# Optimization experiments

Hardware: AMD Instinct MI355X
Metric: run time of the kernel (lower is better)

The kernel has to match this reference:

```python
import jax, jax.numpy as jnp
import numpy as np

B, S = 4, 1024
IN_F, OUT_F = 8192, 8192
ACT_BITS = 8


def setup_inputs() -> dict:
    key = jax.random.key(0)
    k1, k2, k3, k4 = jax.random.split(key, 4)
    x = jax.random.normal(k1, (B, S, IN_F), dtype=jnp.float32)
    # each int8 byte packs two 4-bit exponent nibbles; stored as int32 values in [0, 256)
    packed_exponents = jax.random.randint(k2, (OUT_F, IN_F // 2), 0, 256, dtype=jnp.int32)
    # signs are +/-1 per weight element
    signs = jax.random.randint(k3, (OUT_F, IN_F), 0, 2, dtype=jnp.int32) * 2 - 1
    bias = jax.random.normal(k4, (OUT_F,), dtype=jnp.float32)
    activation_scale = jnp.float32(0.02)  # delta_lsb for int8 activation quant
    min_exp = -14  # python int constant (buffer min_exp in the torch module)
    return {
        "x": x,
        "packed_exponents": packed_exponents,
        "signs": signs,
        "bias": bias,
        "activation_scale": activation_scale,
        "min_exp": min_exp,
    }


def reference(x, packed_exponents, signs, bias, activation_scale, min_exp):
    q_max = 2 ** (ACT_BITS - 1) - 1   # 127
    q_min = -2 ** (ACT_BITS - 1)      # -128
    orig_shape = x.shape
    x2 = x.reshape(-1, orig_shape[-1])  # [N, IN_F]

    # int8 activation quantization (kept in float; values are exact small ints)
    a_quant = jnp.clip(jnp.round(x2 / activation_scale), q_min, q_max)

    # unpack two 4-bit exponent nibbles per byte: low nibble first, then high
    lo = packed_exponents & 0xF
    hi = (packed_exponents >> 4) & 0xF
    exps = jnp.stack([lo, hi], axis=-1).reshape(OUT_F, IN_F)  # [OUT_F, IN_F]

    # dequantized log-domain weights: sign * 2^(nibble + min_exp)
    w = signs.astype(jnp.float32) * jnp.exp2((exps + min_exp).astype(jnp.float32))

    # batched matvec (the CUDA kernel does one row of this per launch) + dequant + bias
    out = (a_quant @ w.T) * activation_scale + bias  # [N, OUT_F]
    return out.reshape(*orig_shape[:-1], OUT_F)
```

## Files before the change

### kernel.cpp

```cpp
#include <hip/hip_runtime.h>
#include <hip/hip_bf16.h>
#include <stdint.h>

#define N_TOK 4096
#define KF    8192
#define NF    8192

#define BM 256
#define BN 256
#define NT (KF / 64)
#define NKH (KF / 32)

typedef __attribute__((ext_vector_type(8))) short short8;
typedef __attribute__((ext_vector_type(4))) float f32x4;

#define GLOBAL_P(p) ((const __attribute__((address_space(1))) void*)(p))
#define LDS_P(p)    ((__attribute__((address_space(3))) void*)(p))

__global__ void quant_x(const float* __restrict__ x, const float* __restrict__ scale_p,
                        uint16_t* __restrict__ a) {
    const float s = *scale_p;
    const int n8 = N_TOK * KF / 8;
    const int stride = gridDim.x * blockDim.x;
    for (int i = blockIdx.x * blockDim.x + threadIdx.x; i < n8; i += stride) {
        const float4* xp = (const float4*)(x + (size_t)i * 8);
        float4 v0 = xp[0], v1 = xp[1];
        float q[8] = {v0.x, v0.y, v0.z, v0.w, v1.x, v1.y, v1.z, v1.w};
        union { uint16_t u16[8]; short8 v; } o;
        #pragma unroll
        for (int j = 0; j < 8; ++j) {
            float t = rintf(q[j] / s);
            t = fminf(fmaxf(t, -128.f), 127.f);
            union { float f; uint32_t u; } cv; cv.f = t;
            o.u16[j] = (uint16_t)(cv.u >> 16);
        }
        *(short8*)(a + (size_t)i * 8) = o.v;
    }
}

__global__ void dequant_w(const int* __restrict__ packed, const int* __restrict__ signs,
                          const int* __restrict__ minexp_p, uint16_t* __restrict__ w) {
    const int me = *minexp_p;
    const int ebase = (me + 127) << 7;
    const int n4 = NF * (KF / 2) / 4;
    const int stride = gridDim.x * blockDim.x;
    for (int i = blockIdx.x * blockDim.x + threadIdx.x; i < n4; i += stride) {
        int4 p  = ((const int4*)packed)[i];
        int4 s0 = ((const int4*)signs)[(size_t)i * 2];
        int4 s1 = ((const int4*)signs)[(size_t)i * 2 + 1];
        int pw[4] = {p.x, p.y, p.z, p.w};
        int sg[8] = {s0.x, s0.y, s0.z, s0.w, s1.x, s1.y, s1.z, s1.w};
        union { uint16_t u16[8]; short8 v; } o;
        #pragma unroll
        for (int j = 0; j < 4; ++j) {
            int lo = pw[j] & 0xF, hi = (pw[j] >> 4) & 0xF;
            o.u16[2 * j]     = (uint16_t)((ebase + (lo << 7)) | (sg[2 * j]     < 0 ? 0x8000 : 0));
            o.u16[2 * j + 1] = (uint16_t)((ebase + (hi << 7)) | (sg[2 * j + 1] < 0 ? 0x8000 : 0));
        }
        *(short8*)(w + (size_t)i * 8) = o.v;
    }
}

#define BARRIER()  asm volatile("s_barrier" ::: "memory")
#define WAITLGKM() asm volatile("s_waitcnt lgkmcnt(0)" ::: "memory")
#define WAITVM8()  asm volatile("s_waitcnt vmcnt(8)" ::: "memory")
#define WAITVM4()  asm volatile("s_waitcnt vmcnt(4)" ::: "memory")
#define WAITVM0()  asm volatile("s_waitcnt vmcnt(0)" ::: "memory")

__global__ __launch_bounds__(512, 2) void gemm_bt(
        const uint16_t* __restrict__ A, const uint16_t* __restrict__ W,
        const float* __restrict__ bias, const float* __restrict__ scale_p,
        float* __restrict__ out) {
    __shared__ uint16_t ldsA[4 * 256 * 32];
    __shared__ uint16_t ldsB[4 * 256 * 32];

    const int tid  = threadIdx.x;
    const int wid  = tid >> 6, lane = tid & 63;
    const int wr = wid >> 2, wc = wid & 3;
    const int rlane = lane & 15, kgrp = lane >> 4;

    const int bid = blockIdx.x;
    const int xcd = bid & 7;
    const int i_l = bid >> 3;
    const int gen = i_l >> 5;
    const int il  = i_l & 31;
    const int by  = gen * 8 + (il >> 2);
    const int bx  = xcd * 4 + (il & 3);
    const int rowA0 = by * BM;
    const int colB0 = bx * BN;

    const int o0 = tid * 16, o1 = (512 + tid) * 16;
    const int l0 = o0 ^ (((o0 >> 9) & 1) << 5);
    const int l1 = o1 ^ (((o1 >> 9) & 1) << 5);
    const char* gA0 = (const char*)A + ((size_t)(rowA0 + (l0 >> 6)) * KF) * 2 + (l0 & 63);
    const char* gA1 = (const char*)A + ((size_t)(rowA0 + (l1 >> 6)) * KF) * 2 + (l1 & 63);
    const char* gB0 = (const char*)W + ((size_t)(colB0 + (l0 >> 6)) * KF) * 2 + (l0 & 63);
    const char* gB1 = (const char*)W + ((size_t)(colB0 + (l1 >> 6)) * KF) * 2 + (l1 & 63);
    const int ldst0 = wid * 1024;
    const int ldst1 = 8192 + wid * 1024;

    int aoff[8], boff[4];
    #pragma unroll
    for (int i = 0; i < 8; ++i) {
        int row = wr * 128 + i * 16 + rlane;
        int o = row * 64 + kgrp * 16;
        aoff[i] = o ^ (((o >> 9) & 1) << 5);
    }
    #pragma unroll
    for (int n = 0; n < 4; ++n) {
        int row = wc * 64 + n * 16 + rlane;
        int o = row * 64 + kgrp * 16;
        boff[n] = o ^ (((o >> 9) & 1) << 5);
    }

#define STAGE_A(j) do { \
    char* b_ = (char*)ldsA + ((j) & 3) * 16384; \
    __builtin_amdgcn_global_load_lds(GLOBAL_P(gA0 + (size_t)(j) * 64), LDS_P(b_ + ldst0), 16, 0, 0); \
    __builtin_amdgcn_global_load_lds(GLOBAL_P(gA1 + (size_t)(j) * 64), LDS_P(b_ + ldst1), 16, 0, 0); \
} while (0)
#define STAGE_B(j) do { \
    char* b_ = (char*)ldsB + ((j) & 3) * 16384; \
    __builtin_amdgcn_global_load_lds(GLOBAL_P(gB0 + (size_t)(j) * 64), LDS_P(b_ + ldst0), 16, 0, 0); \
    __builtin_amdgcn_global_load_lds(GLOBAL_P(gB1 + (size_t)(j) * 64), LDS_P(b_ + ldst1), 16, 0, 0); \
} while (0)
#define LDA(h, slot) do { \
    const char* pa_ = (const char*)ldsA + (slot) * 16384; \
    _Pragma("unroll") for (int mm_ = 0; mm_ < 4; ++mm_) \
        afr[mm_] = *(const short8*)(pa_ + aoff[(h) * 4 + mm_]); \
} while (0)
#define LDB(slot) do { \
    const char* pb_ = (const char*)ldsB + (slot) * 16384; \
    _Pragma("unroll") for (int nn_ = 0; nn_ < 4; ++nn_) \
        bfr[nn_] = *(const short8*)(pb_ + boff[nn_]); \
} while (0)
#define MFMA_HALF(h) do { \
    __builtin_amdgcn_s_setprio(1); \
    _Pragma("unroll") for (int mm_ = 0; mm_ < 4; ++mm_) \
        _Pragma("unroll") for (int nn_ = 0; nn_ < 4; ++nn_) \
            acc[(h) * 4 + mm_][nn_] = __builtin_amdgcn_mfma_f32_16x16x32_bf16( \
                afr[mm_], bfr[nn_], acc[(h) * 4 + mm_][nn_], 0, 0, 0); \
    __builtin_amdgcn_s_setprio(0); \
} while (0)

    f32x4 acc[8][4] = {};
    short8 afr[4], bfr[4];

    STAGE_A(0); STAGE_B(0);
    STAGE_A(1); STAGE_B(1);
    STAGE_A(2); STAGE_B(2);
    WAITVM8();
    BARRIER();

    for (int t = 0; t < NT - 1; ++t) {
        const int j0 = 2 * t;
        const int s0 = j0 & 3, s1 = (j0 + 1) & 3;
        const bool g3 = (j0 + 3) < NKH;
        const bool g4 = (j0 + 4) < NKH;

        LDA(0, s0); LDB(s0);
        if (g3) STAGE_A(j0 + 3);
        BARRIER(); WAITLGKM();
        MFMA_HALF(0);
        BARRIER();
        LDA(1, s0);
        if (g3) STAGE_B(j0 + 3);
        BARRIER(); WAITLGKM();
        MFMA_HALF(1);
        WAITVM8();
        BARRIER();
        LDA(0, s1); LDB(s1);
        if (g4) STAGE_A(j0 + 4);
        BARRIER(); WAITLGKM();
        MFMA_HALF(0);
        BARRIER();
        LDA(1, s1);
        if (g4) STAGE_B(j0 + 4);
        BARRIER(); WAITLGKM();
        MFMA_HALF(1);
        if (t == NT - 2) { WAITVM4(); } else { WAITVM8(); }
        BARRIER();
    }

    {
        LDA(0, 2); LDB(2);
        BARRIER(); WAITLGKM();
        MFMA_HALF(0);
        BARRIER();
        LDA(1, 2);
        BARRIER(); WAITLGKM();
        MFMA_HALF(1);
        WAITVM0();
        BARRIER();
        LDA(0, 3); LDB(3);
        BARRIER(); WAITLGKM();
        MFMA_HALF(0);
        BARRIER();
        LDA(1, 3);
        WAITLGKM();
        MFMA_HALF(1);
    }

    const float s = *scale_p;
    const int colbase = colB0 + wc * 64 + rlane;
    const int rowbase = rowA0 + wr * 128 + kgrp * 4;
    #pragma unroll
    for (int n = 0; n < 4; ++n) {
        const float bv = bias[colbase + n * 16];
        #pragma unroll
        for (int mf = 0; mf < 8; ++mf) {
            #pragma unroll
            for (int r = 0; r < 4; ++r)
                out[(size_t)(rowbase + mf * 16 + r) * NF + colbase + n * 16] = acc[mf][n][r] * s + bv;
        }
    }
#undef STAGE_A
#undef STAGE_B
#undef LDA
#undef LDB
#undef MFMA_HALF
}

extern "C" void kernel_launch(void* const* d_in, const int* in_sizes, int n_in,
                              void* d_out, int out_size, void* d_ws, size_t ws_size,
                              hipStream_t stream) {
    const float* x      = (const float*)d_in[0];
    const int*   packed = (const int*)d_in[1];
    const int*   signs  = (const int*)d_in[2];
    const float* bias   = (const float*)d_in[3];
    const float* scale  = (const float*)d_in[4];
    const int*   minexp = (const int*)d_in[5];
    float* out = (float*)d_out;

    uint16_t* A = (uint16_t*)d_ws;
    uint16_t* W = (uint16_t*)((char*)d_ws + (size_t)N_TOK * KF * 2);

    quant_x<<<2048, 256, 0, stream>>>(x, scale, A);
    dequant_w<<<2048, 256, 0, stream>>>(packed, signs, minexp, W);
    gemm_bt<<<(N_TOK / BM) * (NF / BN), 512, 0, stream>>>(A, W, bias, scale, out);
}
```

Before: 677.8 us.

## Double-buffer LDS fragment registers to overlap LDS reads with MFMA

After: 610.4 us. 9.9% less time.

```diff
diff --git a/kernel.cpp b/kernel.cpp
--- a/kernel.cpp
+++ b/kernel.cpp
@@ -62,10 +62,11 @@
 }
 
 #define BARRIER()  asm volatile("s_barrier" ::: "memory")
-#define WAITLGKM() asm volatile("s_waitcnt lgkmcnt(0)" ::: "memory")
 #define WAITVM8()  asm volatile("s_waitcnt vmcnt(8)" ::: "memory")
 #define WAITVM4()  asm volatile("s_waitcnt vmcnt(4)" ::: "memory")
 #define WAITVM0()  asm volatile("s_waitcnt vmcnt(0)" ::: "memory")
+#define SP1 __builtin_amdgcn_s_setprio(1)
+#define SP0 __builtin_amdgcn_s_setprio(0)
 
 __global__ __launch_bounds__(512, 2) void gemm_bt(
         const uint16_t* __restrict__ A, const uint16_t* __restrict__ W,
@@ -123,82 +124,61 @@
     __builtin_amdgcn_global_load_lds(GLOBAL_P(gB0 + (size_t)(j) * 64), LDS_P(b_ + ldst0), 16, 0, 0); \
     __builtin_amdgcn_global_load_lds(GLOBAL_P(gB1 + (size_t)(j) * 64), LDS_P(b_ + ldst1), 16, 0, 0); \
 } while (0)
-#define LDA(h, slot) do { \
-    const char* pa_ = (const char*)ldsA + (slot) * 16384; \
-    _Pragma("unroll") for (int mm_ = 0; mm_ < 4; ++mm_) \
-        afr[mm_] = *(const short8*)(pa_ + aoff[(h) * 4 + mm_]); \
-} while (0)
-#define LDB(slot) do { \
-    const char* pb_ = (const char*)ldsB + (slot) * 16384; \
-    _Pragma("unroll") for (int nn_ = 0; nn_ < 4; ++nn_) \
-        bfr[nn_] = *(const short8*)(pb_ + boff[nn_]); \
-} while (0)
-#define MFMA_HALF(h) do { \
-    __builtin_amdgcn_s_setprio(1); \
+#define LDA4(DST, H, SLOT) do { \
+    const char* p_ = (const char*)ldsA + (SLOT) * 16384; \
+    _Pragma("unroll") for (int i_ = 0; i_ < 4; ++i_) \
+        DST[i_] = *(const short8*)(p_ + aoff[(H) * 4 + i_]); \
+} while (0)
+#define LDB4(DST, SLOT) do { \
+    const char* p_ = (const char*)ldsB + (SLOT) * 16384; \
+    _Pragma("unroll") for (int i_ = 0; i_ < 4; ++i_) \
+        DST[i_] = *(const short8*)(p_ + boff[i_]); \
+} while (0)
+#define MFMA16(H, AF, BF) do { \
+    SP1; \
     _Pragma("unroll") for (int mm_ = 0; mm_ < 4; ++mm_) \
         _Pragma("unroll") for (int nn_ = 0; nn_ < 4; ++nn_) \
-            acc[(h) * 4 + mm_][nn_] = __builtin_amdgcn_mfma_f32_16x16x32_bf16( \
-                afr[mm_], bfr[nn_], acc[(h) * 4 + mm_][nn_], 0, 0, 0); \
-    __builtin_amdgcn_s_setprio(0); \
+            acc[(H) * 4 + mm_][nn_] = __builtin_amdgcn_mfma_f32_16x16x32_bf16( \
+                AF[mm_], BF[nn_], acc[(H) * 4 + mm_][nn_], 0, 0, 0); \
+    SP0; \
+} while (0)
+
+#define TILE(S0, S1, S0N, ST0, ST1, ST2, ST3, VM0, VM2) do { \
+    BARRIER(); VM0; LDA4(afrY, 1, S0);                 ST0; MFMA16(0, afrX, bfrE); \
+    BARRIER();      LDA4(afrX, 0, S1); LDB4(bfrO, S1); ST1; MFMA16(1, afrY, bfrE); \
+    BARRIER(); VM2; LDA4(afrY, 1, S1);                 ST2; MFMA16(0, afrX, bfrO); \
+    BARRIER();      LDA4(afrX, 0, S0N); LDB4(bfrE, S0N); ST3; MFMA16(1, afrY, bfrO); \
 } while (0)
 
     f32x4 acc[8][4] = {};
-    short8 afr[4], bfr[4];
+    short8 afrX[4], afrY[4], bfrE[4], bfrO[4];
 
     STAGE_A(0); STAGE_B(0);
     STAGE_A(1); STAGE_B(1);
     STAGE_A(2); STAGE_B(2);
     WAITVM8();
     BARRIER();
-
-    for (int t = 0; t < NT - 1; ++t) {
-        const int j0 = 2 * t;
-        const int s0 = j0 & 3, s1 = (j0 + 1) & 3;
-        const bool g3 = (j0 + 3) < NKH;
-        const bool g4 = (j0 + 4) < NKH;
-
-        LDA(0, s0); LDB(s0);
-        if (g3) STAGE_A(j0 + 3);
-        BARRIER(); WAITLGKM();
-        MFMA_HALF(0);
-        BARRIER();
-        LDA(1, s0);
-        if (g3) STAGE_B(j0 + 3);
-        BARRIER(); WAITLGKM();
-        MFMA_HALF(1);
-        WAITVM8();
-        BARRIER();
-        LDA(0, s1); LDB(s1);
-        if (g4) STAGE_A(j0 + 4);
-        BARRIER(); WAITLGKM();
-        MFMA_HALF(0);
-        BARRIER();
-        LDA(1, s1);
-        if (g4) STAGE_B(j0 + 4);
-        BARRIER(); WAITLGKM();
-        MFMA_HALF(1);
-        if (t == NT - 2) { WAITVM4(); } else { WAITVM8(); }
-        BARRIER();
-    }
-
-    {
-        LDA(0, 2); LDB(2);
-        BARRIER(); WAITLGKM();
-        MFMA_HALF(0);
-        BARRIER();
-        LDA(1, 2);
-        BARRIER(); WAITLGKM();
-        MFMA_HALF(1);
-        WAITVM0();
-        BARRIER();
-        LDA(0, 3); LDB(3);
-        BARRIER(); WAITLGKM();
-        MFMA_HALF(0);
-        BARRIER();
-        LDA(1, 3);
-        WAITLGKM();
-        MFMA_HALF(1);
-    }
+    LDA4(afrX, 0, 0);
+    LDB4(bfrE, 0);
+
+    for (int kt2 = 0; kt2 < 63; ++kt2) {
+        const int j0 = kt2 * 4;
+        TILE(0, 1, 2,
+             STAGE_A(j0 + 3), STAGE_B(j0 + 3), STAGE_A(j0 + 4), STAGE_B(j0 + 4),
+             WAITVM4(), WAITVM4());
+        TILE(2, 3, 0,
+             STAGE_A(j0 + 5), STAGE_B(j0 + 5), STAGE_A(j0 + 6), STAGE_B(j0 + 6),
+             WAITVM4(), WAITVM4());
+    }
+
+    TILE(0, 1, 2,
+         STAGE_A(255), STAGE_B(255), (void)0, (void)0,
+         WAITVM4(), WAITVM4());
+
+    BARRIER(); WAITVM0(); LDA4(afrY, 1, 2); MFMA16(0, afrX, bfrE);
+    BARRIER(); LDA4(afrX, 0, 3); LDB4(bfrO, 3); MFMA16(1, afrY, bfrE);
+    BARRIER(); LDA4(afrY, 1, 3); MFMA16(0, afrX, bfrO);
+    BARRIER(); MFMA16(1, afrY, bfrO);
 
     const float s = *scale_p;
     const int colbase = colB0 + wc * 64 + rlane;
@@ -215,9 +195,10 @@
     }
 #undef STAGE_A
 #undef STAGE_B
-#undef LDA
-#undef LDB
-#undef MFMA_HALF
+#undef LDA4
+#undef LDB4
+#undef MFMA16
+#undef TILE
 }
 
 extern "C" void kernel_launch(void* const* d_in, const int* in_sizes, int n_in,
```
